# Kernel optimization log

Hardware: AMD Instinct MI355X
Metric: run time of the kernel (lower is better)

The kernel has to match this reference:

```python
import jax, jax.numpy as jnp
import numpy as np

# MXFP4 e2m1 value lookup (sign bit is the high bit of the nibble)
FP4_LUT = jnp.array([0.0, 0.5, 1.0, 1.5, 2.0, 3.0, 4.0, 6.0,
                     -0.0, -0.5, -1.0, -1.5, -2.0, -3.0, -4.0, -6.0], dtype=jnp.float32)
BLOCK = 32  # mxfp4 scale block size
TOP_K = 2


def dequant_mxfp4(blocks, scales):
    # blocks: [..., K//2] packed uint8 nibbles (low nibble = even elem, high = odd)
    # scales: [..., K//BLOCK] e8m0 biased exponents; scale = 2**(s - 127)
    b = blocks.astype(jnp.int32)
    lo = b & 0xF
    hi = (b >> 4) & 0xF
    nib = jnp.stack([lo, hi], axis=-1).reshape(blocks.shape[:-1] + (blocks.shape[-1] * 2,))
    vals = FP4_LUT[nib]                                   # [..., K]
    s = jnp.exp2(scales.astype(jnp.float32) - 127.0)      # [..., K//BLOCK]
    s = jnp.repeat(s, BLOCK, axis=-1)                     # [..., K]
    return vals * s


def setup_inputs() -> dict:
    key = jax.random.key(0)
    ks = jax.random.split(key, 8)
    E, H, F, B, S = 16, 1024, 2048, 1, 128
    hidden_states = jax.random.normal(ks[0], (B, S, H), dtype=jnp.float32)
    router_w = jax.random.normal(ks[1], (E, H), dtype=jnp.float32) * 0.05
    blocks_gu = jax.random.randint(ks[2], (E, 2 * F, H // 2), 0, 256, dtype=jnp.int32)
    scales_gu = jax.random.randint(ks[3], (E, 2 * F, H // BLOCK), 118, 130, dtype=jnp.int32)
    bias_gu = jax.random.normal(ks[4], (E, 2 * F), dtype=jnp.float32) * 0.02
    blocks_down = jax.random.randint(ks[5], (E, H, F // 2), 0, 256, dtype=jnp.int32)
    scales_down = jax.random.randint(ks[6], (E, H, F // BLOCK), 118, 130, dtype=jnp.int32)
    bias_down = jax.random.normal(ks[7], (E, H), dtype=jnp.float32) * 0.02
    return {"hidden_states": hidden_states, "router_w": router_w,
            "bias_gu": bias_gu, "bias_down": bias_down,
            "blocks_gu": blocks_gu, "scales_gu": scales_gu,
            "blocks_down": blocks_down, "scales_down": scales_down}


def reference(hidden_states, router_w, bias_gu, bias_down,
              blocks_gu, scales_gu, blocks_down, scales_down):
    B, S, H = hidden_states.shape
    flat = hidden_states.reshape(-1, H)                   # [T, H]
    T = flat.shape[0]
    E = router_w.shape[0]

    # --- routing: topk_then_softmax (default softmax_order) ---
    logits = flat @ router_w.T                            # [T, E]
    top_vals, top_idx = jax.lax.top_k(logits, TOP_K)      # [T, K]
    weights = jax.nn.softmax(top_vals, axis=-1).astype(flat.dtype)
    combine = jnp.zeros((T, E), flat.dtype).at[jnp.arange(T)[:, None], top_idx].set(weights)

    # --- mxfp4 dequant of fused expert weights ---
    w_gu = dequant_mxfp4(blocks_gu, scales_gu)            # [E, 2F, H]
    w_down = dequant_mxfp4(blocks_down, scales_down)      # [E, H, F]

    # --- expert MLP (SwiGLU), combined with routing weights ---
    gu = jnp.einsum('th,eoh->eto', flat, w_gu) + bias_gu[:, None, :]   # [E, T, 2F]
    gate, up = jnp.split(gu, 2, axis=-1)
    h = jax.nn.silu(gate) * up                            # [E, T, F]
    y = jnp.einsum('etf,ehf->eth', h, w_down) + bias_down[:, None, :]  # [E, T, H]
    out = jnp.einsum('eth,te->th', y, combine)            # [T, H]
    return out.reshape(B, S, H)
```

## Files before the change

kernel.cpp:

```cpp
#include <hip/hip_runtime.h>
#include <hip/hip_fp16.h>
#include <math.h>

#define NE 16
#define HD 1024
#define FD 2048

typedef _Float16 half8 __attribute__((ext_vector_type(8)));
typedef float f32x4 __attribute__((ext_vector_type(4)));

#define TOPI_OFF 0
#define TOPW_OFF 256
#define CNT_OFF  512
#define PREF_OFF 528
#define SLOT_OFF 544
#define INVT_OFF 800
#define META_OFF 1056
#define TL1_OFF  1060
#define HBUF_OFF 4096
#define Y0_OFF   (HBUF_OFF + 262144)
#define Y1_OFF   (Y0_OFF + 262144)

union XI { int4 v; half8 h; };

#define BARRIER_LDS() asm volatile("s_waitcnt lgkmcnt(0)\ns_barrier" ::: "memory")

__device__ __forceinline__ int fp4h(int nib) {
    int c = nib & 7;
    int v;
    if (c == 0) v = 0;
    else if (c == 1) v = 14 << 10;
    else v = (((c >> 1) + 14) << 10) | ((c & 1) << 9);
    v |= (nib & 8) << 12;
    return v;
}

__device__ __forceinline__ int dec2i(const int* lut, int byte, int sv) {
    int l = lut[byte & 255];
    __half2 p = *reinterpret_cast<const __half2*>(&l);
    __half2 sc = *reinterpret_cast<const __half2*>(&sv);
    __half2 r = __hmul2(p, sc);
    return *reinterpret_cast<int*>(&r);
}

__device__ __forceinline__ void stageB(const int* lut, int4* Bbuf, int rs, int kq,
                                       int4 q0, int4 q1, int sc) {
    int sv = (sc - 112) << 10; sv |= sv << 16;
    int4 o0, o1;
    o0.x = dec2i(lut, q0.x, sv); o0.y = dec2i(lut, q0.y, sv);
    o0.z = dec2i(lut, q0.z, sv); o0.w = dec2i(lut, q0.w, sv);
    o1.x = dec2i(lut, q1.x, sv); o1.y = dec2i(lut, q1.y, sv);
    o1.z = dec2i(lut, q1.z, sv); o1.w = dec2i(lut, q1.w, sv);
    Bbuf[rs * 8 + ((kq * 2) ^ (rs & 7))] = o0;
    Bbuf[rs * 8 + ((kq * 2 + 1) ^ (rs & 7))] = o1;
}

__device__ __forceinline__ void stageA1(int4* Abuf, int a2idx, int4 av) {
    union { int4 v; float f[4]; } uf; uf.v = av;
    union { _Float16 h[4]; int2 p; } o;
    o.h[0] = (_Float16)uf.f[0]; o.h[1] = (_Float16)uf.f[1];
    o.h[2] = (_Float16)uf.f[2]; o.h[3] = (_Float16)uf.f[3];
    ((int2*)Abuf)[a2idx] = o.p;
}

__global__ void routing_kernel(const float* __restrict__ x, const float* __restrict__ rw,
                               int* __restrict__ top_idx, float* __restrict__ top_w) {
    int t = blockIdx.x;
    int tid = threadIdx.x;
    int e = tid >> 4, seg = tid & 15;
    const float4* xr = (const float4*)(x + t * HD + seg * 64);
    const float4* wr = (const float4*)(rw + e * HD + seg * 64);
    float p = 0.f;
    #pragma unroll
    for (int i = 0; i < 16; ++i) {
        float4 a = xr[i], b = wr[i];
        p = fmaf(a.x, b.x, fmaf(a.y, b.y, fmaf(a.z, b.z, fmaf(a.w, b.w, p))));
    }
    __shared__ float part[16][16];
    __shared__ float logit[16];
    part[e][seg] = p;
    __syncthreads();
    if (tid < 16) {
        float s = 0.f;
        #pragma unroll
        for (int i = 0; i < 16; ++i) s += part[tid][i];
        logit[tid] = s;
    }
    __syncthreads();
    if (tid == 0) {
        int i0 = 0; float v0 = logit[0];
        #pragma unroll
        for (int i = 1; i < 16; ++i) { if (logit[i] > v0) { v0 = logit[i]; i0 = i; } }
        int i1 = -1; float v1 = -1e30f;
        #pragma unroll
        for (int i = 0; i < 16; ++i) { if (i != i0 && logit[i] > v1) { v1 = logit[i]; i1 = i; } }
        float w0 = 1.f / (1.f + expf(v1 - v0));
        float w1 = 1.f / (1.f + expf(v0 - v1));
        top_idx[t * 2]     = i0;  top_w[t * 2]     = w0;
        top_idx[t * 2 + 1] = i1;  top_w[t * 2 + 1] = w1;
    }
}

__global__ void build_kernel(const int* __restrict__ top_idx,
                             int* __restrict__ cnt, int* __restrict__ pref,
                             int* __restrict__ slot, int* __restrict__ invtok,
                             int* __restrict__ meta, int* __restrict__ tl1) {
    __shared__ int scnt[16], spref[16], scur[16];
    int tid = threadIdx.x;
    if (tid < 16) scnt[tid] = 0;
    __syncthreads();
    int e = top_idx[tid];
    atomicAdd(&scnt[e], 1);
    __syncthreads();
    if (tid == 0) {
        int s = 0;
        for (int i = 0; i < 16; ++i) { spref[i] = s; pref[i] = s; cnt[i] = scnt[i]; s += scnt[i]; }
        int m1 = 0;
        for (int i = 0; i < 16; ++i) {
            int ntile1 = (scnt[i] + 15) >> 4;
            for (int m = 0; m < ntile1; ++m) tl1[m1++] = (i << 8) | m;
        }
        meta[0] = m1;
    }
    if (tid < 16) scur[tid] = 0;
    __syncthreads();
    int pos = spref[e] + atomicAdd(&scur[e], 1);
    slot[tid] = pos;
    invtok[pos] = tid >> 1;
}

__global__ __launch_bounds__(256) void gemm1_mfma(
    const float* __restrict__ x, const int* __restrict__ invtok,
    const int* __restrict__ qblk, const int* __restrict__ qscl,
    const float* __restrict__ bias,
    const int* __restrict__ cnt, const int* __restrict__ pref,
    const int* __restrict__ meta, const int* __restrict__ tl1,
    _Float16* __restrict__ hbuf) {
    __shared__ int lut[256];
    __shared__ int4 Asb[2][128];
    __shared__ int4 Bsb[2][512];
    __shared__ float exch[4][64][4];
    int tid = threadIdx.x;
    lut[tid] = fp4h(tid & 15) | (fp4h(tid >> 4) << 16);
    int wave = tid >> 6, lane = tid & 63;
    int bl = lane & 15, kb4 = lane >> 4;
    int rloc = wave * 16 + bl;
    int rs = tid >> 2, kq = tid & 3;
    int tok = tid >> 4, jj = tid & 15;
    int a2idx = (tok * 8 + ((jj >> 1) ^ (tok & 7))) * 2 + (jj & 1);
    int nwork = meta[0] << 6;

    for (int w = blockIdx.x; w < nwork; w += gridDim.x) {
        int tile = tl1[w >> 6];
        int fc = w & 63;
        int e = tile >> 8, mt = tile & 255;
        int n = cnt[e];
        int nt = n - mt * 16; if (nt > 16) nt = 16;
        int base = pref[e];
        int t0 = base + mt * 16;
        int f0 = fc * 32;

        long rowg = (long)e * 4096 + ((rs < 32) ? (f0 + rs) : (2048 + f0 + rs - 32));
        const int4* wrow = (const int4*)(qblk + rowg * 512);
        const int* srow = qscl + rowg * 32;
        int gtok = invtok[t0 + ((tok < nt) ? tok : nt - 1)];
        const int4* arow = (const int4*)x + (long)gtok * 256;

        int4 c0q0 = wrow[kq * 2], c0q1 = wrow[kq * 2 + 1];
        int  c0sc = srow[kq >> 1];
        int4 c0av = arow[jj];
        __syncthreads();
        stageA1(Asb[0], a2idx, c0av);
        stageB(lut, Bsb[0], rs, kq, c0q0, c0q1, c0sc);
        int4 aq0 = wrow[8 + kq * 2], aq1 = wrow[8 + kq * 2 + 1];
        int  asc = srow[2 + (kq >> 1)];
        int4 aav = arow[16 + jj];
        int4 bq0 = wrow[16 + kq * 2], bq1 = wrow[16 + kq * 2 + 1];
        int  bsc = srow[4 + (kq >> 1)];
        int4 bav = arow[32 + jj];
        BARRIER_LDS();

        f32x4 acc = {0.f, 0.f, 0.f, 0.f};
        #pragma unroll
        for (int p = 0; p < 8; ++p) {
            int kb = 2 * p;
            #pragma unroll
            for (int ks = 0; ks < 2; ++ks) {
                int g = ks * 4 + kb4;
                XI a, b;
                a.v = Asb[0][bl * 8 + (g ^ (bl & 7))];
                b.v = Bsb[0][rloc * 8 + (g ^ (rloc & 7))];
                acc = __builtin_amdgcn_mfma_f32_16x16x32_f16(a.h, b.h, acc, 0, 0, 0);
            }
            stageA1(Asb[1], a2idx, aav);
            stageB(lut, Bsb[1], rs, kq, aq0, aq1, asc);
            if (p < 7) {
                int s = kb + 3;
                aq0 = wrow[s * 8 + kq * 2]; aq1 = wrow[s * 8 + kq * 2 + 1];
                asc = srow[s * 2 + (kq >> 1)];
                aav = arow[s * 16 + jj];
            }
            BARRIER_LDS();
            #pragma unroll
            for (int ks = 0; ks < 2; ++ks) {
                int g = ks * 4 + kb4;
                XI a, b;
                a.v = Asb[1][bl * 8 + (g ^ (bl & 7))];
                b.v = Bsb[1][rloc * 8 + (g ^ (rloc & 7))];
                acc = __builtin_amdgcn_mfma_f32_16x16x32_f16(a.h, b.h, acc, 0, 0, 0);
            }
            if (p < 7) {
                stageA1(Asb[0], a2idx, bav);
                stageB(lut, Bsb[0], rs, kq, bq0, bq1, bsc);
                if (p < 6) {
                    int s = kb + 4;
                    bq0 = wrow[s * 8 + kq * 2]; bq1 = wrow[s * 8 + kq * 2 + 1];
                    bsc = srow[s * 2 + (kq >> 1)];
                    bav = arow[s * 16 + jj];
                }
            }
            BARRIER_LDS();
        }
        #pragma unroll
        for (int i = 0; i < 4; ++i) exch[wave][lane][i] = acc[i];
        __syncthreads();
        int fl = tid & 31, wv = fl >> 4, col = fl & 15;
        float bg = bias[(long)e * 4096 + f0 + fl];
        float bu = bias[(long)e * 4096 + 2048 + f0 + fl];
        #pragma unroll
        for (int d = 0; d < 2; ++d) {
            int tk = (tid >> 5) + d * 8;
            int ln = ((tk >> 2) << 4) | col;
            int rg = tk & 3;
            float g = exch[wv][ln][rg] + bg;
            float u = exch[wv + 2][ln][rg] + bu;
            float h = (g / (1.f + expf(-g))) * u;
            if (tk < nt)
                hbuf[(long)(t0 + tk) * FD + f0 + fl] = (_Float16)(h * 0.0625f);
        }
        __syncthreads();
    }
}

__global__ __launch_bounds__(256) void gemm2_mfma(
    const _Float16* __restrict__ hbuf, const int* __restrict__ qblk,
    const int* __restrict__ qscl, const float* __restrict__ bias,
    const int* __restrict__ cnt, const int* __restrict__ pref,
    const int* __restrict__ meta, const int* __restrict__ tl1,
    float* __restrict__ y0p, float* __restrict__ y1p) {
    __shared__ int lut[256];
    __shared__ int4 Asb[2][128];
    __shared__ int4 Bsb[2][512];
    int tid = threadIdx.x;
    lut[tid] = fp4h(tid & 15) | (fp4h(tid >> 4) << 16);
    int wave = tid >> 6, lane = tid & 63;
    int bl = lane & 15, kb4 = lane >> 4;
    int rloc = wave * 16 + bl;
    int rs = tid >> 2, kq = tid & 3;
    int tok = tid >> 3, ga = tid & 7;
    int aidx = tok * 8 + (ga ^ (tok & 7));
    int nwork = meta[0] << 5;

    for (int w = blockIdx.x; w < nwork; w += gridDim.x) {
        int tile = tl1[w >> 5];
        int sub = w & 31;
        int hc = sub & 15, kh = sub >> 4;
        int e = tile >> 8, mt = tile & 255;
        int n = cnt[e];
        int nt = n - mt * 16; if (nt > 16) nt = 16;
        int base = pref[e];
        int t0 = base + mt * 16;
        int h0 = hc * 64;

        long rowg = (long)e * HD + h0 + rs;
        const int4* wrow = (const int4*)(qblk + rowg * 1024) + (kh * 16) * 8;
        const int* srow = qscl + rowg * 64 + kh * 32;
        int tclamp = (tok < nt) ? tok : nt - 1;
        const int4* arow = (const int4*)hbuf + (long)(t0 + tclamp) * 256 + (kh * 16) * 8;

        int4 c0q0 = wrow[kq * 2], c0q1 = wrow[kq * 2 + 1];
        int  c0sc = srow[kq >> 1];
        int4 c0av;
        if (tid < 128) c0av = arow[ga];
        __syncthreads();
        if (tid < 128) Asb[0][aidx] = c0av;
        stageB(lut, Bsb[0], rs, kq, c0q0, c0q1, c0sc);
        int4 aq0 = wrow[8 + kq * 2], aq1 = wrow[8 + kq * 2 + 1];
        int  asc = srow[2 + (kq >> 1)];
        int4 aav; if (tid < 128) aav = arow[8 + ga];
        int4 bq0 = wrow[16 + kq * 2], bq1 = wrow[16 + kq * 2 + 1];
        int  bsc = srow[4 + (kq >> 1)];
        int4 bav; if (tid < 128) bav = arow[16 + ga];
        BARRIER_LDS();

        f32x4 acc = {0.f, 0.f, 0.f, 0.f};
        #pragma unroll
        for (int p = 0; p < 8; ++p) {
            int kb = 2 * p;
            #pragma unroll
            for (int ks = 0; ks < 2; ++ks) {
                int g = ks * 4 + kb4;
                XI a, b;
                a.v = Asb[0][bl * 8 + (g ^ (bl & 7))];
                b.v = Bsb[0][rloc * 8 + (g ^ (rloc & 7))];
                acc = __builtin_amdgcn_mfma_f32_16x16x32_f16(a.h, b.h, acc, 0, 0, 0);
            }
            if (tid < 128) Asb[1][aidx] = aav;
            stageB(lut, Bsb[1], rs, kq, aq0, aq1, asc);
            if (p < 7) {
                int s = kb + 3;
                aq0 = wrow[s * 8 + kq * 2]; aq1 = wrow[s * 8 + kq * 2 + 1];
                asc = srow[s * 2 + (kq >> 1)];
                if (tid < 128) aav = arow[s * 8 + ga];
            }
            BARRIER_LDS();
            #pragma unroll
            for (int ks = 0; ks < 2; ++ks) {
                int g = ks * 4 + kb4;
                XI a, b;
                a.v = Asb[1][bl * 8 + (g ^ (bl & 7))];
                b.v = Bsb[1][rloc * 8 + (g ^ (rloc & 7))];
                acc = __builtin_amdgcn_mfma_f32_16x16x32_f16(a.h, b.h, acc, 0, 0, 0);
            }
            if (p < 7) {
                if (tid < 128) Asb[0][aidx] = bav;
                stageB(lut, Bsb[0], rs, kq, bq0, bq1, bsc);
                if (p < 6) {
                    int s = kb + 4;
                    bq0 = wrow[s * 8 + kq * 2]; bq1 = wrow[s * 8 + kq * 2 + 1];
                    bsc = srow[s * 2 + (kq >> 1)];
                    if (tid < 128) bav = arow[s * 8 + ga];
                }
            }
            BARRIER_LDS();
        }
        int hcol = h0 + wave * 16 + bl;
        float bv = (kh == 0) ? bias[(long)e * HD + hcol] : 0.f;
        float* yp = (kh == 0) ? y0p : y1p;
        #pragma unroll
        for (int r = 0; r < 4; ++r) {
            int row = kb4 * 4 + r;
            if (row < nt)
                yp[(long)(t0 + row) * HD + hcol] = acc[r] * 16.f + bv;
        }
        __syncthreads();
    }
}

__global__ void combine_kernel(const float* __restrict__ y0, const float* __restrict__ y1,
                               const int* __restrict__ slot, const float* __restrict__ topw,
                               float* __restrict__ out) {
    int t = blockIdx.x;
    int i = threadIdx.x;
    int s0 = slot[2 * t], s1 = slot[2 * t + 1];
    float w0 = topw[2 * t], w1 = topw[2 * t + 1];
    float4 a0 = ((const float4*)(y0 + (long)s0 * HD))[i];
    float4 a1 = ((const float4*)(y1 + (long)s0 * HD))[i];
    float4 b0 = ((const float4*)(y0 + (long)s1 * HD))[i];
    float4 b1 = ((const float4*)(y1 + (long)s1 * HD))[i];
    float4 o;
    o.x = w0 * (a0.x + a1.x) + w1 * (b0.x + b1.x);
    o.y = w0 * (a0.y + a1.y) + w1 * (b0.y + b1.y);
    o.z = w0 * (a0.z + a1.z) + w1 * (b0.z + b1.z);
    o.w = w0 * (a0.w + a1.w) + w1 * (b0.w + b1.w);
    ((float4*)(out + (long)t * HD))[i] = o;
}

extern "C" void kernel_launch(void* const* d_in, const int* in_sizes, int n_in,
                              void* d_out, int out_size, void* d_ws, size_t ws_size,
                              hipStream_t stream) {
    const float* x          = (const float*)d_in[0];
    const float* rw         = (const float*)d_in[1];
    const float* bias_gu    = (const float*)d_in[2];
    const float* bias_down  = (const float*)d_in[3];
    const int*   blocks_gu  = (const int*)d_in[4];
    const int*   scales_gu  = (const int*)d_in[5];
    const int*   blocks_down= (const int*)d_in[6];
    const int*   scales_down= (const int*)d_in[7];
    float* out = (float*)d_out;
    int*   wsI = (int*)d_ws;
    float* wsF = (float*)d_ws;
    _Float16* hbuf = (_Float16*)(wsI + HBUF_OFF);
    float*    y0   = wsF + Y0_OFF;
    float*    y1   = wsF + Y1_OFF;

    routing_kernel<<<128, 256, 0, stream>>>(x, rw, wsI + TOPI_OFF, wsF + TOPW_OFF);
    build_kernel<<<1, 256, 0, stream>>>(wsI + TOPI_OFF, wsI + CNT_OFF, wsI + PREF_OFF,
                                        wsI + SLOT_OFF, wsI + INVT_OFF,
                                        wsI + META_OFF, wsI + TL1_OFF);
    gemm1_mfma<<<2048, 256, 0, stream>>>(x, wsI + INVT_OFF, blocks_gu, scales_gu, bias_gu,
                                         wsI + CNT_OFF, wsI + PREF_OFF,
                                         wsI + META_OFF, wsI + TL1_OFF, hbuf);
    gemm2_mfma<<<1024, 256, 0, stream>>>(hbuf, blocks_down, scales_down, bias_down,
                                         wsI + CNT_OFF, wsI + PREF_OFF,
                                         wsI + META_OFF, wsI + TL1_OFF, y0, y1);
    combine_kernel<<<128, 256, 0, stream>>>(y0, y1, wsI + SLOT_OFF, wsF + TOPW_OFF, out);
}
```

Before: 57.67 us.

## Widen token tile to 32 rows in both expert GEMMs to reuse dequantized weights

Token tiles per expert grow from 16 to 32 rows. Each block now issues two MFMAs per staged weight fragment with two accumulators, so every dequantized FP4 weight tile in LDS serves twice as many tokens. This is meant to halve the number of tiles and the repeated weight loading and dequantization when an expert has more than 16 tokens. In exchange LDS use and register pressure grow, experts with 16 or fewer tokens waste half the MFMA work, and the grid sizes are halved to match.

After: 55.53 us. 3.7% less time.

```diff
diff --git a/kernel.cpp b/kernel.cpp
--- a/kernel.cpp
+++ b/kernel.cpp
@@ -55,12 +55,14 @@
     Bbuf[rs * 8 + ((kq * 2 + 1) ^ (rs & 7))] = o1;
 }
 
-__device__ __forceinline__ void stageA1(int4* Abuf, int a2idx, int4 av) {
-    union { int4 v; float f[4]; } uf; uf.v = av;
-    union { _Float16 h[4]; int2 p; } o;
-    o.h[0] = (_Float16)uf.f[0]; o.h[1] = (_Float16)uf.f[1];
-    o.h[2] = (_Float16)uf.f[2]; o.h[3] = (_Float16)uf.f[3];
-    ((int2*)Abuf)[a2idx] = o.p;
+__device__ __forceinline__ void stageA2(int4* Abuf, int aidx, int4 av0, int4 av1) {
+    union { int4 v; float f[4]; } u0, u1; u0.v = av0; u1.v = av1;
+    union { _Float16 h[8]; int4 p; } o;
+    o.h[0] = (_Float16)u0.f[0]; o.h[1] = (_Float16)u0.f[1];
+    o.h[2] = (_Float16)u0.f[2]; o.h[3] = (_Float16)u0.f[3];
+    o.h[4] = (_Float16)u1.f[0]; o.h[5] = (_Float16)u1.f[1];
+    o.h[6] = (_Float16)u1.f[2]; o.h[7] = (_Float16)u1.f[3];
+    Abuf[aidx] = o.p;
 }
 
 __global__ void routing_kernel(const float* __restrict__ x, const float* __restrict__ rw,
@@ -117,8 +119,8 @@
         for (int i = 0; i < 16; ++i) { spref[i] = s; pref[i] = s; cnt[i] = scnt[i]; s += scnt[i]; }
         int m1 = 0;
         for (int i = 0; i < 16; ++i) {
-            int ntile1 = (scnt[i] + 15) >> 4;
-            for (int m = 0; m < ntile1; ++m) tl1[m1++] = (i << 8) | m;
+            int ntile = (scnt[i] + 31) >> 5;
+            for (int m = 0; m < ntile; ++m) tl1[m1++] = (i << 8) | m;
         }
         meta[0] = m1;
     }
@@ -137,17 +139,17 @@
     const int* __restrict__ meta, const int* __restrict__ tl1,
     _Float16* __restrict__ hbuf) {
     __shared__ int lut[256];
-    __shared__ int4 Asb[2][128];
+    __shared__ int4 Asb[2][256];
     __shared__ int4 Bsb[2][512];
-    __shared__ float exch[4][64][4];
+    __shared__ float exch[4][64][8];
     int tid = threadIdx.x;
     lut[tid] = fp4h(tid & 15) | (fp4h(tid >> 4) << 16);
     int wave = tid >> 6, lane = tid & 63;
     int bl = lane & 15, kb4 = lane >> 4;
     int rloc = wave * 16 + bl;
     int rs = tid >> 2, kq = tid & 3;
-    int tok = tid >> 4, jj = tid & 15;
-    int a2idx = (tok * 8 + ((jj >> 1) ^ (tok & 7))) * 2 + (jj & 1);
+    int tokA = tid >> 3, ja = tid & 7;
+    int aidx = tokA * 8 + (ja ^ (tokA & 7));
     int nwork = meta[0] << 6;
 
     for (int w = blockIdx.x; w < nwork; w += gridDim.x) {
@@ -155,83 +157,91 @@
         int fc = w & 63;
         int e = tile >> 8, mt = tile & 255;
         int n = cnt[e];
-        int nt = n - mt * 16; if (nt > 16) nt = 16;
+        int nt = n - mt * 32; if (nt > 32) nt = 32;
         int base = pref[e];
-        int t0 = base + mt * 16;
+        int t0 = base + mt * 32;
         int f0 = fc * 32;
 
         long rowg = (long)e * 4096 + ((rs < 32) ? (f0 + rs) : (2048 + f0 + rs - 32));
         const int4* wrow = (const int4*)(qblk + rowg * 512);
         const int* srow = qscl + rowg * 32;
-        int gtok = invtok[t0 + ((tok < nt) ? tok : nt - 1)];
+        int gtok = invtok[t0 + ((tokA < nt) ? tokA : nt - 1)];
         const int4* arow = (const int4*)x + (long)gtok * 256;
 
         int4 c0q0 = wrow[kq * 2], c0q1 = wrow[kq * 2 + 1];
         int  c0sc = srow[kq >> 1];
-        int4 c0av = arow[jj];
+        int4 c0a0 = arow[ja * 2], c0a1 = arow[ja * 2 + 1];
         __syncthreads();
-        stageA1(Asb[0], a2idx, c0av);
+        stageA2(Asb[0], aidx, c0a0, c0a1);
         stageB(lut, Bsb[0], rs, kq, c0q0, c0q1, c0sc);
         int4 aq0 = wrow[8 + kq * 2], aq1 = wrow[8 + kq * 2 + 1];
         int  asc = srow[2 + (kq >> 1)];
-        int4 aav = arow[16 + jj];
+        int4 aa0 = arow[16 + ja * 2], aa1 = arow[16 + ja * 2 + 1];
         int4 bq0 = wrow[16 + kq * 2], bq1 = wrow[16 + kq * 2 + 1];
         int  bsc = srow[4 + (kq >> 1)];
-        int4 bav = arow[32 + jj];
+        int4 ba0 = arow[32 + ja * 2], ba1 = arow[32 + ja * 2 + 1];
         BARRIER_LDS();
 
-        f32x4 acc = {0.f, 0.f, 0.f, 0.f};
+        f32x4 acc0 = {0.f, 0.f, 0.f, 0.f}, acc1 = {0.f, 0.f, 0.f, 0.f};
         #pragma unroll
         for (int p = 0; p < 8; ++p) {
             int kb = 2 * p;
             #pragma unroll
             for (int ks = 0; ks < 2; ++ks) {
                 int g = ks * 4 + kb4;
-                XI a, b;
-                a.v = Asb[0][bl * 8 + (g ^ (bl & 7))];
+                XI a0, a1, b;
                 b.v = Bsb[0][rloc * 8 + (g ^ (rloc & 7))];
-                acc = __builtin_amdgcn_mfma_f32_16x16x32_f16(a.h, b.h, acc, 0, 0, 0);
-            }
-            stageA1(Asb[1], a2idx, aav);
+                a0.v = Asb[0][bl * 8 + (g ^ (bl & 7))];
+                a1.v = Asb[0][(16 + bl) * 8 + (g ^ (bl & 7))];
+                acc0 = __builtin_amdgcn_mfma_f32_16x16x32_f16(a0.h, b.h, acc0, 0, 0, 0);
+                acc1 = __builtin_amdgcn_mfma_f32_16x16x32_f16(a1.h, b.h, acc1, 0, 0, 0);
+            }
+            stageA2(Asb[1], aidx, aa0, aa1);
             stageB(lut, Bsb[1], rs, kq, aq0, aq1, asc);
             if (p < 7) {
                 int s = kb + 3;
                 aq0 = wrow[s * 8 + kq * 2]; aq1 = wrow[s * 8 + kq * 2 + 1];
                 asc = srow[s * 2 + (kq >> 1)];
-                aav = arow[s * 16 + jj];
+                aa0 = arow[s * 16 + ja * 2]; aa1 = arow[s * 16 + ja * 2 + 1];
             }
             BARRIER_LDS();
             #pragma unroll
             for (int ks = 0; ks < 2; ++ks) {
                 int g = ks * 4 + kb4;
-                XI a, b;
-                a.v = Asb[1][bl * 8 + (g ^ (bl & 7))];
+                XI a0, a1, b;
                 b.v = Bsb[1][rloc * 8 + (g ^ (rloc & 7))];
-                acc = __builtin_amdgcn_mfma_f32_16x16x32_f16(a.h, b.h, acc, 0, 0, 0);
+                a0.v = Asb[1][bl * 8 + (g ^ (bl & 7))];
+                a1.v = Asb[1][(16 + bl) * 8 + (g ^ (bl & 7))];
+                acc0 = __builtin_amdgcn_mfma_f32_16x16x32_f16(a0.h, b.h, acc0, 0, 0, 0);
+                acc1 = __builtin_amdgcn_mfma_f32_16x16x32_f16(a1.h, b.h, acc1, 0, 0, 0);
             }
             if (p < 7) {
-                stageA1(Asb[0], a2idx, bav);
+                stageA2(Asb[0], aidx, ba0, ba1);
                 stageB(lut, Bsb[0], rs, kq, bq0, bq1, bsc);
                 if (p < 6) {
                     int s = kb + 4;
                     bq0 = wrow[s * 8 + kq * 2]; bq1 = wrow[s * 8 + kq * 2 + 1];
                     bsc = srow[s * 2 + (kq >> 1)];
-                    bav = arow[s * 16 + jj];
+                    ba0 = arow[s * 16 + ja * 2]; ba1 = arow[s * 16 + ja * 2 + 1];
                 }
             }
             BARRIER_LDS();
         }
         #pragma unroll
-        for (int i = 0; i < 4; ++i) exch[wave][lane][i] = acc[i];
+        for (int i = 0; i < 4; ++i) {
+            exch[wave][lane][i] = acc0[i];
+            exch[wave][lane][4 + i] = acc1[i];
+        }
         __syncthreads();
         int fl = tid & 31, wv = fl >> 4, col = fl & 15;
         float bg = bias[(long)e * 4096 + f0 + fl];
         float bu = bias[(long)e * 4096 + 2048 + f0 + fl];
         #pragma unroll
-        for (int d = 0; d < 2; ++d) {
+        for (int d = 0; d < 4; ++d) {
             int tk = (tid >> 5) + d * 8;
-            int ln = ((tk >> 2) << 4) | col;
-            int rg = tk & 3;
+            int tr = tk & 15;
+            int ln = ((tr >> 2) << 4) | col;
+            int rg = (tr & 3) + ((tk >= 16) ? 4 : 0);
             float g = exch[wv][ln][rg] + bg;
             float u = exch[wv + 2][ln][rg] + bu;
             float h = (g / (1.f + expf(-g))) * u;
@@ -249,7 +259,7 @@
     const int* __restrict__ meta, const int* __restrict__ tl1,
     float* __restrict__ y0p, float* __restrict__ y1p) {
     __shared__ int lut[256];
-    __shared__ int4 Asb[2][128];
+    __shared__ int4 Asb[2][256];
     __shared__ int4 Bsb[2][512];
     int tid = threadIdx.x;
     lut[tid] = fp4h(tid & 15) | (fp4h(tid >> 4) << 16);
@@ -257,8 +267,8 @@
     int bl = lane & 15, kb4 = lane >> 4;
     int rloc = wave * 16 + bl;
     int rs = tid >> 2, kq = tid & 3;
-    int tok = tid >> 3, ga = tid & 7;
-    int aidx = tok * 8 + (ga ^ (tok & 7));
+    int tokA = tid >> 3, ga = tid & 7;
+    int aidx = tokA * 8 + (ga ^ (tokA & 7));
     int nwork = meta[0] << 5;
 
     for (int w = blockIdx.x; w < nwork; w += gridDim.x) {
@@ -267,69 +277,72 @@
         int hc = sub & 15, kh = sub >> 4;
         int e = tile >> 8, mt = tile & 255;
         int n = cnt[e];
-        int nt = n - mt * 16; if (nt > 16) nt = 16;
+        int nt = n - mt * 32; if (nt > 32) nt = 32;
         int base = pref[e];
-        int t0 = base + mt * 16;
+        int t0 = base + mt * 32;
         int h0 = hc * 64;
 
         long rowg = (long)e * HD + h0 + rs;
         const int4* wrow = (const int4*)(qblk + rowg * 1024) + (kh * 16) * 8;
         const int* srow = qscl + rowg * 64 + kh * 32;
-        int tclamp = (tok < nt) ? tok : nt - 1;
-        const int4* arow = (const int4*)hbuf + (long)(t0 + tclamp) * 256 + (kh * 16) * 8;
+        int tclamp = (tokA < nt) ? tokA : nt - 1;
+        const int4* arow = (const int4*)hbuf + (long)(t0 + tclamp) * 256 + kh * 128;
 
         int4 c0q0 = wrow[kq * 2], c0q1 = wrow[kq * 2 + 1];
         int  c0sc = srow[kq >> 1];
-        int4 c0av;
-        if (tid < 128) c0av = arow[ga];
+        int4 c0av = arow[ga];
         __syncthreads();
-        if (tid < 128) Asb[0][aidx] = c0av;
+        Asb[0][aidx] = c0av;
         stageB(lut, Bsb[0], rs, kq, c0q0, c0q1, c0sc);
         int4 aq0 = wrow[8 + kq * 2], aq1 = wrow[8 + kq * 2 + 1];
         int  asc = srow[2 + (kq >> 1)];
-        int4 aav; if (tid < 128) aav = arow[8 + ga];
+        int4 aav = arow[8 + ga];
         int4 bq0 = wrow[16 + kq * 2], bq1 = wrow[16 + kq * 2 + 1];
         int  bsc = srow[4 + (kq >> 1)];
-        int4 bav; if (tid < 128) bav = arow[16 + ga];
+        int4 bav = arow[16 + ga];
         BARRIER_LDS();
 
-        f32x4 acc = {0.f, 0.f, 0.f, 0.f};
+        f32x4 acc0 = {0.f, 0.f, 0.f, 0.f}, acc1 = {0.f, 0.f, 0.f, 0.f};
         #pragma unroll
         for (int p = 0; p < 8; ++p) {
             int kb = 2 * p;
             #pragma unroll
             for (int ks = 0; ks < 2; ++ks) {
                 int g = ks * 4 + kb4;
-                XI a, b;
-                a.v = Asb[0][bl * 8 + (g ^ (bl & 7))];
+                XI a0, a1, b;
                 b.v = Bsb[0][rloc * 8 + (g ^ (rloc & 7))];
-                acc = __builtin_amdgcn_mfma_f32_16x16x32_f16(a.h, b.h, acc, 0, 0, 0);
-            }
-            if (tid < 128) Asb[1][aidx] = aav;
+                a0.v = Asb[0][bl * 8 + (g ^ (bl & 7))];
+                a1.v = Asb[0][(16 + bl) * 8 + (g ^ (bl & 7))];
+                acc0 = __builtin_amdgcn_mfma_f32_16x16x32_f16(a0.h, b.h, acc0, 0, 0, 0);
+                acc1 = __builtin_amdgcn_mfma_f32_16x16x32_f16(a1.h, b.h, acc1, 0, 0, 0);
+            }
+            Asb[1][aidx] = aav;
             stageB(lut, Bsb[1], rs, kq, aq0, aq1, asc);
             if (p < 7) {
                 int s = kb + 3;
                 aq0 = wrow[s * 8 + kq * 2]; aq1 = wrow[s * 8 + kq * 2 + 1];
                 asc = srow[s * 2 + (kq >> 1)];
-                if (tid < 128) aav = arow[s * 8 + ga];
+                aav = arow[s * 8 + ga];
             }
             BARRIER_LDS();
             #pragma unroll
             for (int ks = 0; ks < 2; ++ks) {
                 int g = ks * 4 + kb4;
-                XI a, b;
-                a.v = Asb[1][bl * 8 + (g ^ (bl & 7))];
+                XI a0, a1, b;
                 b.v = Bsb[1][rloc * 8 + (g ^ (rloc & 7))];
-                acc = __builtin_amdgcn_mfma_f32_16x16x32_f16(a.h, b.h, acc, 0, 0, 0);
+                a0.v = Asb[1][bl * 8 + (g ^ (bl & 7))];
+                a1.v = Asb[1][(16 + bl) * 8 + (g ^ (bl & 7))];
+                acc0 = __builtin_amdgcn_mfma_f32_16x16x32_f16(a0.h, b.h, acc0, 0, 0, 0);
+                acc1 = __builtin_amdgcn_mfma_f32_16x16x32_f16(a1.h, b.h, acc1, 0, 0, 0);
             }
             if (p < 7) {
-                if (tid < 128) Asb[0][aidx] = bav;
+                Asb[0][aidx] = bav;
                 stageB(lut, Bsb[0], rs, kq, bq0, bq1, bsc);
                 if (p < 6) {
                     int s = kb + 4;
                     bq0 = wrow[s * 8 + kq * 2]; bq1 = wrow[s * 8 + kq * 2 + 1];
                     bsc = srow[s * 2 + (kq >> 1)];
-                    if (tid < 128) bav = arow[s * 8 + ga];
+                    bav = arow[s * 8 + ga];
                 }
             }
             BARRIER_LDS();
@@ -339,9 +352,12 @@
         float* yp = (kh == 0) ? y0p : y1p;
         #pragma unroll
         for (int r = 0; r < 4; ++r) {
-            int row = kb4 * 4 + r;
-            if (row < nt)
-                yp[(long)(t0 + row) * HD + hcol] = acc[r] * 16.f + bv;
+            int row0 = kb4 * 4 + r;
+            if (row0 < nt)
+                yp[(long)(t0 + row0) * HD + hcol] = acc0[r] * 16.f + bv;
+            int row1 = 16 + kb4 * 4 + r;
+            if (row1 < nt)
+                yp[(long)(t0 + row1) * HD + hcol] = acc1[r] * 16.f + bv;
         }
         __syncthreads();
     }
@@ -388,11 +404,11 @@
     build_kernel<<<1, 256, 0, stream>>>(wsI + TOPI_OFF, wsI + CNT_OFF, wsI + PREF_OFF,
                                         wsI + SLOT_OFF, wsI + INVT_OFF,
                                         wsI + META_OFF, wsI + TL1_OFF);
-    gemm1_mfma<<<2048, 256, 0, stream>>>(x, wsI + INVT_OFF, blocks_gu, scales_gu, bias_gu,
+    gemm1_mfma<<<1024, 256, 0, stream>>>(x, wsI + INVT_OFF, blocks_gu, scales_gu, bias_gu,
                                          wsI + CNT_OFF, wsI + PREF_OFF,
                                          wsI + META_OFF, wsI + TL1_OFF, hbuf);
-    gemm2_mfma<<<1024, 256, 0, stream>>>(hbuf, blocks_down, scales_down, bias_down,
-                                         wsI + CNT_OFF, wsI + PREF_OFF,
-                                         wsI + META_OFF, wsI + TL1_OFF, y0, y1);
+    gemm2_mfma<<<512, 256, 0, stream>>>(hbuf, blocks_down, scales_down, bias_down,
+                                        wsI + CNT_OFF, wsI + PREF_OFF,
+                                        wsI + META_OFF, wsI + TL1_OFF, y0, y1);
     combine_kernel<<<128, 256, 0, stream>>>(y0, y1, wsI + SLOT_OFF, wsF + TOPW_OFF, out);
 }
```
